# Kernel optimization log

Hardware: AMD Instinct MI355X
Metric: run time of the kernel (lower is better)

## Reference

```python
import jax, jax.numpy as jnp
import numpy as np

T, B, IN, H, OUT = 512, 256, 64, 512, 64


def setup_inputs() -> dict:
    key = jax.random.key(0)
    ks = jax.random.split(key, 12)
    s_in = 1.0 / np.sqrt(H)
    u = lambda k, shape: jax.random.uniform(k, shape, jnp.float32, -s_in, s_in)
    return {
        "x": jax.random.normal(ks[0], (T, B, IN), jnp.float32),
        # layer 0 LSTMCell params (PyTorch layout: [4H, in], gate order i,f,g,o)
        "W_ih0": u(ks[1], (4 * H, IN)),
        "W_hh0": u(ks[2], (4 * H, H)),
        "b_ih0": u(ks[3], (4 * H,)),
        "b_hh0": u(ks[4], (4 * H,)),
        # layer 1 LSTMCell params
        "W_ih1": u(ks[5], (4 * H, H)),
        "W_hh1": u(ks[6], (4 * H, H)),
        "b_ih1": u(ks[7], (4 * H,)),
        "b_hh1": u(ks[8], (4 * H,)),
        # output linear
        "W_lin": u(ks[9], (OUT, H)),
        "b_lin": u(ks[10], (OUT,)),
        "future": 0,
    }


def _lstm_cell(x_t, h, c, Wi, Wh, bi, bh):
    # gates: [B, 4H], PyTorch order i, f, g, o
    g = x_t @ Wi.T + bi + h @ Wh.T + bh
    i, f, gg, o = jnp.split(g, 4, axis=-1)
    c_new = jax.nn.sigmoid(f) * c + jax.nn.sigmoid(i) * jnp.tanh(gg)
    h_new = jax.nn.sigmoid(o) * jnp.tanh(c_new)
    return h_new, c_new


def reference(x, W_ih0, W_hh0, b_ih0, b_hh0, W_ih1, W_hh1, b_ih1, b_hh1,
              W_lin, b_lin, future):
    Bs = x.shape[1]
    h0 = jnp.zeros((Bs, H), x.dtype)
    init = (h0, h0, h0, h0)  # h_t[0], c_t[0], h_t[1], c_t[1]

    def step(carry, x_t):
        h_0, c_0, h_1, c_1 = carry
        h_0, c_0 = _lstm_cell(x_t, h_0, c_0, W_ih0, W_hh0, b_ih0, b_hh0)
        h_1, c_1 = _lstm_cell(h_0, h_1, c_1, W_ih1, W_hh1, b_ih1, b_hh1)
        out = h_1 @ W_lin.T + b_lin  # dropout is identity in eval mode
        return (h_0, c_0, h_1, c_1), out

    carry, outs = jax.lax.scan(step, init, x)  # outs: [T, B, OUT]

    if future > 0:
        def fstep(state, _):
            (h_0, c_0, h_1, c_1), out = state
            h_0, c_0 = _lstm_cell(out, h_0, c_0, W_ih0, W_hh0, b_ih0, b_hh0)
            h_1, c_1 = _lstm_cell(h_0, h_1, c_1, W_ih1, W_hh1, b_ih1, b_hh1)
            out = h_1 @ W_lin.T + b_lin
            return ((h_0, c_0, h_1, c_1), out), out
        _, fouts = jax.lax.scan(fstep, (carry, outs[-1]), None, length=future)
        outs = jnp.concatenate([outs, fouts], axis=0)

    # torch.cat(outputs, dim=1): [B, (T+future)*OUT]
    return jnp.transpose(outs, (1, 0, 2)).reshape(Bs, -1)
```

## Files before the change

### kernel.cpp

```cpp
#include <hip/hip_runtime.h>
#include <hip/hip_bf16.h>

#define TT  512
#define BB  256
#define IND 64
#define HH  512
#define OD  64
#define BBHH (BB * HH)
#define NSLOT 8
#define FSTRIDE 32
#define XSTR  133
#define XSTR0 261

typedef __bf16 v8bf  __attribute__((ext_vector_type(8)));
typedef float  v4f   __attribute__((ext_vector_type(4)));
typedef float  v16f  __attribute__((ext_vector_type(16)));


struct Params {
  const __bf16 *xb, *Wi0, *Wh0, *Wi1, *Wh1, *Wlin;
  const float  *bsum0, *bsum1, *blin;
  __bf16 *h0, *h1;
  int *flags;
  float *out;
};

__device__ __forceinline__ float sigm(float x) { return 1.f / (1.f + __expf(-x)); }
__device__ __forceinline__ float tanh_fast(float x) {
  float e = __expf(2.f * x);
  return 1.f - 2.f / (e + 1.f);
}
__device__ __forceinline__ v4f mfma16(v8bf a, v8bf b, v4f c) {
  return __builtin_amdgcn_mfma_f32_16x16x32_bf16(a, b, c, 0, 0, 0);
}
__device__ __forceinline__ v16f mfma32(v8bf a, v8bf b, v16f c) {
  return __builtin_amdgcn_mfma_f32_32x32x16_bf16(a, b, c, 0, 0, 0);
}
__device__ __forceinline__ v8bf bc(v4f x) { return __builtin_bit_cast(v8bf, x); }

__device__ __forceinline__ void ldsload16(const __bf16* g, __bf16* l) {
  __builtin_amdgcn_global_load_lds(
      (const __attribute__((address_space(1))) void*)(const void*)g,
      (__attribute__((address_space(3))) void*)(void*)l,
      16, 0, 17);
}
__device__ __forceinline__ void vwait() {
  asm volatile("s_waitcnt vmcnt(0)" ::: "memory");
}
__device__ __forceinline__ void astore8(unsigned long long* p, unsigned long long v) {
  __hip_atomic_store(p, v, __ATOMIC_RELAXED, __HIP_MEMORY_SCOPE_AGENT);
}
__device__ __forceinline__ void pollOne(const int* p, int target) {
  while (__hip_atomic_load(p, __ATOMIC_RELAXED, __HIP_MEMORY_SCOPE_AGENT) < target)
    __builtin_amdgcn_s_sleep(1);
}
__device__ __forceinline__ void drainAll() {
  asm volatile("s_waitcnt vmcnt(0)" ::: "memory");
  __syncthreads();
}
__device__ __forceinline__ void setFlag(int* f, int v) {
  if (threadIdx.x == 0)
    __hip_atomic_store(f, v, __ATOMIC_RELAXED, __HIP_MEMORY_SCOPE_AGENT);
}

__global__ void __launch_bounds__(256) prep_kernel(
    const float* x, const float* Wi0, const float* Wh0, const float* bi0, const float* bh0,
    const float* Wi1, const float* Wh1, const float* bi1, const float* bh1, const float* Wlin,
    __bf16* xb, __bf16* Wi0b, __bf16* Wh0b, __bf16* Wi1b, __bf16* Wh1b, __bf16* Wlinb,
    float* bsum0, float* bsum1, __bf16* h0, __bf16* h1, int* flags) {
  size_t tid = (size_t)blockIdx.x * blockDim.x + threadIdx.x;
  size_t np  = (size_t)gridDim.x * blockDim.x;
  for (size_t i = tid; i < (size_t)TT * BB * IND; i += np) xb[i]    = (__bf16)x[i];
  for (size_t i = tid; i < (size_t)4 * HH * IND;  i += np) Wi0b[i]  = (__bf16)Wi0[i];
  for (size_t i = tid; i < (size_t)4 * HH * HH;   i += np) Wh0b[i]  = (__bf16)Wh0[i];
  for (size_t i = tid; i < (size_t)4 * HH * HH;   i += np) Wi1b[i]  = (__bf16)Wi1[i];
  for (size_t i = tid; i < (size_t)4 * HH * HH;   i += np) Wh1b[i]  = (__bf16)Wh1[i];
  for (size_t i = tid; i < (size_t)OD * HH;       i += np) Wlinb[i] = (__bf16)Wlin[i];
  for (size_t i = tid; i < (size_t)4 * HH; i += np) {
    bsum0[i] = bi0[i] + bh0[i];
    bsum1[i] = bi1[i] + bh1[i];
  }
  for (size_t i = tid; i < (size_t)NSLOT * BBHH; i += np) { h0[i] = (__bf16)0.f; h1[i] = (__bf16)0.f; }
  for (size_t i = tid; i < (size_t)200 * FSTRIDE; i += np)
    __hip_atomic_store(&flags[i], 0, __ATOMIC_RELAXED, __HIP_MEMORY_SCOPE_AGENT);
}

__global__ void __launch_bounds__(256, 1) lstm_persist(Params P) {
  __shared__ __align__(16) __bf16 sA[32 * 128 * 8];
  __shared__ __align__(16) float  xch[32 * XSTR0];

  const int bid  = blockIdx.x;
  const int tid  = threadIdx.x;
  const int lane = tid & 63;
  const int wid  = tid >> 6;
  const int khi  = lane >> 5;
  const int l32  = lane & 31;
  const int g    = bid & 7;
  const int k    = bid >> 3;
  int* FL = P.flags;
  const int m0 = g * 32;

  if (k >= 8 && k < 24) {
    const int j  = k - 8;
    const int j0 = j * 32;
    const int n  = wid * HH + j0 + l32;
    v4f breg[64];
    {
      const __bf16* Wh = P.Wh1 + (size_t)n * HH + khi * 8;
      #pragma unroll
      for (int ks = 0; ks < 32; ++ks) breg[ks]      = *(const v4f*)(Wh + ks * 16);
      const __bf16* Wi = P.Wi1 + (size_t)n * HH + khi * 8;
      #pragma unroll
      for (int ks = 0; ks < 32; ++ks) breg[32 + ks] = *(const v4f*)(Wi + ks * 16);
      #pragma unroll
      for (int i = 0; i < 64; ++i) asm volatile("" : "+v"(breg[i]));
    }
    const int er = tid & 31, ecg = tid >> 5;
    const int jc = j0 + ecg * 4;
    const v4f bI = *(const v4f*)(P.bsum1 + jc);
    const v4f bF = *(const v4f*)(P.bsum1 + HH + jc);
    const v4f bG = *(const v4f*)(P.bsum1 + 2 * HH + jc);
    const v4f bO = *(const v4f*)(P.bsum1 + 3 * HH + jc);
    float creg[4] = {0.f, 0.f, 0.f, 0.f};
    const int hsw = l32 & 7;
    const __bf16* abase = sA + (size_t)l32 * 128 * 8;

    for (int t = 0; t < TT; ++t) {
      if (tid < 16)       pollOne(FL + (64 + g * 16 + tid) * FSTRIDE, t);
      else if (tid < 24)  pollOne(FL + (g * 8 + (tid - 16)) * FSTRIDE, t + 1);
      else if (tid == 24) pollOne(FL + (192 + g) * FSTRIDE, t - 7);
      __syncthreads();
      {
        const __bf16* s1 = P.h1 + (size_t)((t + NSLOT - 1) & (NSLOT - 1)) * BBHH + (size_t)m0 * HH;
        const __bf16* s0 = P.h0 + (size_t)(t & (NSLOT - 1)) * BBHH + (size_t)m0 * HH;
        #pragma unroll
        for (int rr = 0; rr < 8; ++rr) {
          const int r  = wid * 8 + rr;
          const int cc = lane ^ (r & 7);
          ldsload16(s1 + (size_t)r * HH + cc * 8, sA + ((size_t)r * 128) * 8);
          ldsload16(s0 + (size_t)r * HH + cc * 8, sA + ((size_t)r * 128 + 64) * 8);
        }
        vwait();
      }
      __syncthreads();
      v16f a0 = {0,0,0,0,0,0,0,0,0,0,0,0,0,0,0,0};
      v16f a1 = {0,0,0,0,0,0,0,0,0,0,0,0,0,0,0,0};
      #pragma unroll
      for (int ks = 0; ks < 64; ks += 2) {
        v8bf af0 = *(const v8bf*)(abase + (((ks    ) * 2 + khi) ^ hsw) * 8);
        a0 = mfma32(af0, bc(breg[ks]), a0);
        v8bf af1 = *(const v8bf*)(abase + (((ks + 1) * 2 + khi) ^ hsw) * 8);
        a1 = mfma32(af1, bc(breg[ks + 1]), a1);
      }
      #pragma unroll
      for (int rg = 0; rg < 16; ++rg) {
        int row = (rg & 3) + 8 * (rg >> 2) + 4 * khi;
        xch[row * XSTR + wid * 32 + l32] = a0[rg] + a1[rg];
      }
      __syncthreads();
      {
        const float* xr = xch + er * XSTR + ecg * 4;
        v4f vi = *(const v4f*)(xr);
        v4f vf = *(const v4f*)(xr + 32);
        v4f vg = *(const v4f*)(xr + 64);
        v4f vo = *(const v4f*)(xr + 96);
        unsigned long long pk = 0;
        #pragma unroll
        for (int q = 0; q < 4; ++q) {
          float cn = sigm(vf[q] + bF[q]) * creg[q] + sigm(vi[q] + bI[q]) * tanh_fast(vg[q] + bG[q]);
          creg[q] = cn;
          __bf16 hb = (__bf16)(sigm(vo[q] + bO[q]) * tanh_fast(cn));
          pk |= (unsigned long long)__builtin_bit_cast(unsigned short, hb) << (16 * q);
        }
        astore8((unsigned long long*)(P.h1 + (size_t)(t & (NSLOT - 1)) * BBHH
                                      + (size_t)(m0 + er) * HH + jc), pk);
      }
      drainAll();
      setFlag(FL + (64 + g * 16 + j) * FSTRIDE, t + 1);
    }
  } else if (k < 8) {
    const int j  = k;
    const int nA = wid * HH + j * 64 + l32;
    const int nB = nA + 32;
    v4f bregA[36], bregB[36];
    {
      const __bf16* WiA = P.Wi0 + (size_t)nA * IND + khi * 8;
      const __bf16* WiB = P.Wi0 + (size_t)nB * IND + khi * 8;
      #pragma unroll
      for (int ks = 0; ks < 4; ++ks) {
        bregA[ks] = *(const v4f*)(WiA + ks * 16);
        bregB[ks] = *(const v4f*)(WiB + ks * 16);
      }
      const __bf16* WhA = P.Wh0 + (size_t)nA * HH + khi * 8;
      const __bf16* WhB = P.Wh0 + (size_t)nB * HH + khi * 8;
      #pragma unroll
      for (int ks = 0; ks < 32; ++ks) {
        bregA[4 + ks] = *(const v4f*)(WhA + ks * 16);
        bregB[4 + ks] = *(const v4f*)(WhB + ks * 16);
      }
      #pragma unroll
      for (int i = 0; i < 36; ++i) {
        asm volatile("" : "+v"(bregA[i]));
        asm volatile("" : "+v"(bregB[i]));
      }
    }
    const int er = tid & 31, ec8 = tid >> 5;
    const int jc = j * 64 + ec8 * 8;
    float creg[8] = {0.f,0.f,0.f,0.f,0.f,0.f,0.f,0.f};
    const int hsw = l32 & 7;
    const __bf16* abase = sA + (size_t)l32 * 72 * 8;

    for (int t = 0; t < TT; ++t) {
      if (tid < 8)       pollOne(FL + (g * 8 + tid) * FSTRIDE, t);
      else if (tid < 24) pollOne(FL + (64 + g * 16 + (tid - 8)) * FSTRIDE, t - 7);
      __syncthreads();
      const __bf16* h0src = P.h0 + (size_t)((t + NSLOT - 1) & (NSLOT - 1)) * BBHH;
      __bf16*       hdst  = P.h0 + (size_t)(t & (NSLOT - 1)) * BBHH;
      {
        const __bf16* hs = h0src + (size_t)m0 * HH;
        #pragma unroll
        for (int rr = 0; rr < 8; ++rr) {
          const int r  = wid * 8 + rr;
          const int cc = lane ^ (r & 7);
          ldsload16(hs + (size_t)r * HH + cc * 8, sA + ((size_t)r * 72 + 8) * 8);
        }
        const int xrow = tid >> 3, xcc = tid & 7;
        v8bf tx = *(const v8bf*)(P.xb + (size_t)t * BB * IND
                                 + (size_t)(m0 + xrow) * IND + xcc * 8);
        *(v8bf*)(sA + ((size_t)xrow * 72 + (xcc ^ (xrow & 7))) * 8) = tx;
        vwait();
      }
      __syncthreads();
      v16f accA = {0,0,0,0,0,0,0,0,0,0,0,0,0,0,0,0};
      v16f accB = {0,0,0,0,0,0,0,0,0,0,0,0,0,0,0,0};
      #pragma unroll
      for (int ks = 0; ks < 36; ++ks) {
        v8bf af = *(const v8bf*)(abase + (((ks << 1) + khi) ^ hsw) * 8);
        accA = mfma32(af, bc(bregA[ks]), accA);
        accB = mfma32(af, bc(bregB[ks]), accB);
      }
      #pragma unroll
      for (int rg = 0; rg < 16; ++rg) {
        int row = (rg & 3) + 8 * (rg >> 2) + 4 * khi;
        xch[row * XSTR0 + wid * 64 + l32]      = accA[rg];
        xch[row * XSTR0 + wid * 64 + 32 + l32] = accB[rg];
      }
      __syncthreads();
      {
        const float* xr = xch + er * XSTR0 + ec8 * 8;
        #pragma unroll
        for (int p = 0; p < 2; ++p) {
          const int cb = jc + p * 4;
          v4f vi = *(const v4f*)(xr + p * 4);
          v4f vf = *(const v4f*)(xr + 64 + p * 4);
          v4f vg = *(const v4f*)(xr + 128 + p * 4);
          v4f vo = *(const v4f*)(xr + 192 + p * 4);
          v4f bI = *(const v4f*)(P.bsum0 + cb);
          v4f bF = *(const v4f*)(P.bsum0 + HH + cb);
          v4f bG = *(const v4f*)(P.bsum0 + 2 * HH + cb);
          v4f bO = *(const v4f*)(P.bsum0 + 3 * HH + cb);
          unsigned long long pk = 0;
          #pragma unroll
          for (int q = 0; q < 4; ++q) {
            float cn = sigm(vf[q] + bF[q]) * creg[p * 4 + q]
                     + sigm(vi[q] + bI[q]) * tanh_fast(vg[q] + bG[q]);
            creg[p * 4 + q] = cn;
            __bf16 hb = (__bf16)(sigm(vo[q] + bO[q]) * tanh_fast(cn));
            pk |= (unsigned long long)__builtin_bit_cast(unsigned short, hb) << (16 * q);
          }
          astore8((unsigned long long*)(hdst + (size_t)(m0 + er) * HH + cb), pk);
        }
      }
      drainAll();
      setFlag(FL + (g * 8 + j) * FSTRIDE, t + 1);
    }
  } else {
    const int l16 = lane & 15, quad = lane >> 4;
    const int col = wid * 16 + l16;
    v4f breg[16];
    {
      const __bf16* W = P.Wlin + (size_t)col * HH + quad * 8;
      #pragma unroll
      for (int kk = 0; kk < 16; ++kk) breg[kk] = *(const v4f*)(W + kk * 32);
      #pragma unroll
      for (int i = 0; i < 16; ++i) asm volatile("" : "+v"(breg[i]));
    }
    const float bb = P.blin[col];
    for (int t = 0; t < TT; ++t) {
      if (tid < 16) pollOne(FL + (64 + g * 16 + tid) * FSTRIDE, t + 1);
      __syncthreads();
      {
        const __bf16* src = P.h1 + (size_t)(t & (NSLOT - 1)) * BBHH + (size_t)m0 * HH;
        #pragma unroll
        for (int rr = 0; rr < 8; ++rr) {
          const int r  = wid * 8 + rr;
          const int cc = lane ^ (r & 7);
          ldsload16(src + (size_t)r * HH + cc * 8, sA + ((size_t)r * 64) * 8);
        }
        vwait();
      }
      __syncthreads();
      setFlag(FL + (192 + g) * FSTRIDE, t + 1);
      v4f acc0 = {0.f,0.f,0.f,0.f}, acc1 = {0.f,0.f,0.f,0.f};
      #pragma unroll
      for (int kk = 0; kk < 16; ++kk) {
        int c8 = kk * 4 + quad;
        int r0 = l16, r1 = 16 + l16;
        v8bf af0 = *(const v8bf*)(sA + ((size_t)r0 * 64 + (c8 ^ (r0 & 7))) * 8);
        acc0 = mfma16(af0, bc(breg[kk]), acc0);
        v8bf af1 = *(const v8bf*)(sA + ((size_t)r1 * 64 + (c8 ^ (r1 & 7))) * 8);
        acc1 = mfma16(af1, bc(breg[kk]), acc1);
      }
      #pragma unroll
      for (int r = 0; r < 4; ++r) {
        int b0r = m0 + quad * 4 + r;
        P.out[(size_t)b0r * (TT * OD) + (size_t)t * OD + col] = acc0[r] + bb;
        int b1r = m0 + 16 + quad * 4 + r;
        P.out[(size_t)b1r * (TT * OD) + (size_t)t * OD + col] = acc1[r] + bb;
      }
    }
  }
}

extern "C" void kernel_launch(void* const* d_in, const int* in_sizes, int n_in,
                              void* d_out, int out_size, void* d_ws, size_t ws_size,
                              hipStream_t stream) {
  const float* x    = (const float*)d_in[0];
  const float* Wi0  = (const float*)d_in[1];
  const float* Wh0  = (const float*)d_in[2];
  const float* bi0  = (const float*)d_in[3];
  const float* bh0  = (const float*)d_in[4];
  const float* Wi1  = (const float*)d_in[5];
  const float* Wh1  = (const float*)d_in[6];
  const float* bi1  = (const float*)d_in[7];
  const float* bh1  = (const float*)d_in[8];
  const float* Wlin = (const float*)d_in[9];
  const float* blin = (const float*)d_in[10];

  char* base = (char*)d_ws;
  size_t off = 0;
  auto take = [&](size_t nbytes) {
    void* p = base + off;
    off = (off + nbytes + 255) & ~(size_t)255;
    return p;
  };
  __bf16* xb    = (__bf16*)take(sizeof(__bf16) * (size_t)TT * BB * IND);
  __bf16* Wi0b  = (__bf16*)take(sizeof(__bf16) * 4 * HH * IND);
  __bf16* Wh0b  = (__bf16*)take(sizeof(__bf16) * 4 * HH * HH);
  __bf16* Wi1b  = (__bf16*)take(sizeof(__bf16) * 4 * HH * HH);
  __bf16* Wh1b  = (__bf16*)take(sizeof(__bf16) * 4 * HH * HH);
  __bf16* Wlinb = (__bf16*)take(sizeof(__bf16) * OD * HH);
  float*  bsum0 = (float*)take(sizeof(float) * 4 * HH);
  float*  bsum1 = (float*)take(sizeof(float) * 4 * HH);
  __bf16* h0    = (__bf16*)take(sizeof(__bf16) * NSLOT * BBHH);
  __bf16* h1    = (__bf16*)take(sizeof(__bf16) * NSLOT * BBHH);
  int*    flags = (int*)take(sizeof(int) * 200 * FSTRIDE);

  prep_kernel<<<dim3(1024), dim3(256), 0, stream>>>(
      x, Wi0, Wh0, bi0, bh0, Wi1, Wh1, bi1, bh1, Wlin,
      xb, Wi0b, Wh0b, Wi1b, Wh1b, Wlinb, bsum0, bsum1, h0, h1, flags);

  Params P;
  P.xb = xb; P.Wi0 = Wi0b; P.Wh0 = Wh0b; P.Wi1 = Wi1b; P.Wh1 = Wh1b; P.Wlin = Wlinb;
  P.bsum0 = bsum0; P.bsum1 = bsum1; P.blin = blin;
  P.h0 = h0; P.h1 = h1;
  P.flags = flags;
  P.out = (float*)d_out;

  void* kargs[] = { (void*)&P };
  hipError_t err = hipLaunchCooperativeKernel(reinterpret_cast<void*>(lstm_persist),
                                              dim3(200), dim3(256), kargs, 0, stream);
  if (err != hipSuccess) {
    lstm_persist<<<dim3(200), dim3(256), 0, stream>>>(P);
  }
}
```

Measured before the change: 3.292 ms.

## Use XCD-local cache scope for h exchange when each group shares one XCD

At startup every block records its XCD id and waits at a grid-wide arrival counter, then checks whether all 25 blocks of its batch group g landed on the same XCD. If so, h loads into LDS use cache policy 1 instead of 17 and h stores use workgroup scope instead of agent scope, so exchanges can stay in the XCD-local L2 and skip device-coherent traffic. Output stores also become nontemporal. The added startup barrier costs some time. Correctness depends on the cache-coherence assumptions holding across CUs within one XCD.

After: 2.945 ms. -10.5%, faster.

```diff
diff --git a/kernel.cpp b/kernel.cpp
--- a/kernel.cpp
+++ b/kernel.cpp
@@ -22,6 +22,8 @@
   const float  *bsum0, *bsum1, *blin;
   __bf16 *h0, *h1;
   int *flags;
+  int *xcdmap;
+  int *ready;
   float *out;
 };
 
@@ -38,17 +40,26 @@
 }
 __device__ __forceinline__ v8bf bc(v4f x) { return __builtin_bit_cast(v8bf, x); }
 
-__device__ __forceinline__ void ldsload16(const __bf16* g, __bf16* l) {
-  __builtin_amdgcn_global_load_lds(
-      (const __attribute__((address_space(1))) void*)(const void*)g,
-      (__attribute__((address_space(3))) void*)(void*)l,
-      16, 0, 17);
+template<bool LOCAL>
+__device__ __forceinline__ void ldsload16T(const __bf16* g, __bf16* l) {
+  if constexpr (LOCAL)
+    __builtin_amdgcn_global_load_lds(
+        (const __attribute__((address_space(1))) void*)(const void*)g,
+        (__attribute__((address_space(3))) void*)(void*)l, 16, 0, 1);
+  else
+    __builtin_amdgcn_global_load_lds(
+        (const __attribute__((address_space(1))) void*)(const void*)g,
+        (__attribute__((address_space(3))) void*)(void*)l, 16, 0, 17);
 }
 __device__ __forceinline__ void vwait() {
   asm volatile("s_waitcnt vmcnt(0)" ::: "memory");
 }
-__device__ __forceinline__ void astore8(unsigned long long* p, unsigned long long v) {
-  __hip_atomic_store(p, v, __ATOMIC_RELAXED, __HIP_MEMORY_SCOPE_AGENT);
+template<bool LOCAL>
+__device__ __forceinline__ void astore8T(unsigned long long* p, unsigned long long v) {
+  if constexpr (LOCAL)
+    __hip_atomic_store(p, v, __ATOMIC_RELAXED, __HIP_MEMORY_SCOPE_WORKGROUP);
+  else
+    __hip_atomic_store(p, v, __ATOMIC_RELAXED, __HIP_MEMORY_SCOPE_AGENT);
 }
 __device__ __forceinline__ void pollOne(const int* p, int target) {
   while (__hip_atomic_load(p, __ATOMIC_RELAXED, __HIP_MEMORY_SCOPE_AGENT) < target)
@@ -67,7 +78,7 @@
     const float* x, const float* Wi0, const float* Wh0, const float* bi0, const float* bh0,
     const float* Wi1, const float* Wh1, const float* bi1, const float* bh1, const float* Wlin,
     __bf16* xb, __bf16* Wi0b, __bf16* Wh0b, __bf16* Wi1b, __bf16* Wh1b, __bf16* Wlinb,
-    float* bsum0, float* bsum1, __bf16* h0, __bf16* h1, int* flags) {
+    float* bsum0, float* bsum1, __bf16* h0, __bf16* h1, int* flags, int* ready) {
   size_t tid = (size_t)blockIdx.x * blockDim.x + threadIdx.x;
   size_t np  = (size_t)gridDim.x * blockDim.x;
   for (size_t i = tid; i < (size_t)TT * BB * IND; i += np) xb[i]    = (__bf16)x[i];
@@ -83,14 +94,12 @@
   for (size_t i = tid; i < (size_t)NSLOT * BBHH; i += np) { h0[i] = (__bf16)0.f; h1[i] = (__bf16)0.f; }
   for (size_t i = tid; i < (size_t)200 * FSTRIDE; i += np)
     __hip_atomic_store(&flags[i], 0, __ATOMIC_RELAXED, __HIP_MEMORY_SCOPE_AGENT);
-}
-
-__global__ void __launch_bounds__(256, 1) lstm_persist(Params P) {
-  __shared__ __align__(16) __bf16 sA[32 * 128 * 8];
-  __shared__ __align__(16) float  xch[32 * XSTR0];
-
-  const int bid  = blockIdx.x;
-  const int tid  = threadIdx.x;
+  if (tid == 0) *ready = 0;
+}
+
+template<bool LOCAL>
+__device__ __forceinline__ void persist_body(const Params& P, int bid, int tid,
+                                             __bf16* sA, float* xch) {
   const int lane = tid & 63;
   const int wid  = tid >> 6;
   const int khi  = lane >> 5;
@@ -137,8 +146,8 @@
         for (int rr = 0; rr < 8; ++rr) {
           const int r  = wid * 8 + rr;
           const int cc = lane ^ (r & 7);
-          ldsload16(s1 + (size_t)r * HH + cc * 8, sA + ((size_t)r * 128) * 8);
-          ldsload16(s0 + (size_t)r * HH + cc * 8, sA + ((size_t)r * 128 + 64) * 8);
+          ldsload16T<LOCAL>(s1 + (size_t)r * HH + cc * 8, sA + ((size_t)r * 128) * 8);
+          ldsload16T<LOCAL>(s0 + (size_t)r * HH + cc * 8, sA + ((size_t)r * 128 + 64) * 8);
         }
         vwait();
       }
@@ -172,8 +181,8 @@
           __bf16 hb = (__bf16)(sigm(vo[q] + bO[q]) * tanh_fast(cn));
           pk |= (unsigned long long)__builtin_bit_cast(unsigned short, hb) << (16 * q);
         }
-        astore8((unsigned long long*)(P.h1 + (size_t)(t & (NSLOT - 1)) * BBHH
-                                      + (size_t)(m0 + er) * HH + jc), pk);
+        astore8T<LOCAL>((unsigned long long*)(P.h1 + (size_t)(t & (NSLOT - 1)) * BBHH
+                                              + (size_t)(m0 + er) * HH + jc), pk);
       }
       drainAll();
       setFlag(FL + (64 + g * 16 + j) * FSTRIDE, t + 1);
@@ -222,7 +231,7 @@
         for (int rr = 0; rr < 8; ++rr) {
           const int r  = wid * 8 + rr;
           const int cc = lane ^ (r & 7);
-          ldsload16(hs + (size_t)r * HH + cc * 8, sA + ((size_t)r * 72 + 8) * 8);
+          ldsload16T<LOCAL>(hs + (size_t)r * HH + cc * 8, sA + ((size_t)r * 72 + 8) * 8);
         }
         const int xrow = tid >> 3, xcc = tid & 7;
         v8bf tx = *(const v8bf*)(P.xb + (size_t)t * BB * IND
@@ -268,7 +277,7 @@
             __bf16 hb = (__bf16)(sigm(vo[q] + bO[q]) * tanh_fast(cn));
             pk |= (unsigned long long)__builtin_bit_cast(unsigned short, hb) << (16 * q);
           }
-          astore8((unsigned long long*)(hdst + (size_t)(m0 + er) * HH + cb), pk);
+          astore8T<LOCAL>((unsigned long long*)(hdst + (size_t)(m0 + er) * HH + cb), pk);
         }
       }
       drainAll();
@@ -295,7 +304,7 @@
         for (int rr = 0; rr < 8; ++rr) {
           const int r  = wid * 8 + rr;
           const int cc = lane ^ (r & 7);
-          ldsload16(src + (size_t)r * HH + cc * 8, sA + ((size_t)r * 64) * 8);
+          ldsload16T<LOCAL>(src + (size_t)r * HH + cc * 8, sA + ((size_t)r * 64) * 8);
         }
         vwait();
       }
@@ -314,12 +323,51 @@
       #pragma unroll
       for (int r = 0; r < 4; ++r) {
         int b0r = m0 + quad * 4 + r;
-        P.out[(size_t)b0r * (TT * OD) + (size_t)t * OD + col] = acc0[r] + bb;
+        __builtin_nontemporal_store(acc0[r] + bb,
+            &P.out[(size_t)b0r * (TT * OD) + (size_t)t * OD + col]);
         int b1r = m0 + 16 + quad * 4 + r;
-        P.out[(size_t)b1r * (TT * OD) + (size_t)t * OD + col] = acc1[r] + bb;
+        __builtin_nontemporal_store(acc1[r] + bb,
+            &P.out[(size_t)b1r * (TT * OD) + (size_t)t * OD + col]);
       }
     }
   }
+}
+
+__global__ void __launch_bounds__(256, 1) lstm_persist(Params P) {
+  __shared__ __align__(16) __bf16 sA[32 * 128 * 8];
+  __shared__ __align__(16) float  xch[32 * XSTR0];
+  __shared__ int sLocal;
+
+  const int bid = blockIdx.x;
+  const int tid = threadIdx.x;
+  const int g   = bid & 7;
+
+  if (tid == 0) {
+    int xcd;
+    asm volatile("s_getreg_b32 %0, hwreg(HW_REG_XCC_ID)" : "=s"(xcd));
+    __hip_atomic_store(&P.xcdmap[bid], xcd, __ATOMIC_RELAXED, __HIP_MEMORY_SCOPE_AGENT);
+    asm volatile("s_waitcnt vmcnt(0)" ::: "memory");
+    asm volatile("buffer_inv sc0 sc1" ::: "memory");
+    __hip_atomic_fetch_add(P.ready, 1, __ATOMIC_RELAXED, __HIP_MEMORY_SCOPE_AGENT);
+    int it = 0;
+    while (__hip_atomic_load(P.ready, __ATOMIC_RELAXED, __HIP_MEMORY_SCOPE_AGENT) < 200
+           && it < 200000) {
+      __builtin_amdgcn_s_sleep(2);
+      ++it;
+    }
+    int ok = (it < 200000) ? 1 : 0;
+    if (ok) {
+      int x0 = __hip_atomic_load(&P.xcdmap[g], __ATOMIC_RELAXED, __HIP_MEMORY_SCOPE_AGENT);
+      for (int kk = 1; kk < 25; ++kk)
+        ok &= (__hip_atomic_load(&P.xcdmap[g + 8 * kk], __ATOMIC_RELAXED,
+                                 __HIP_MEMORY_SCOPE_AGENT) == x0);
+    }
+    sLocal = ok;
+  }
+  __syncthreads();
+
+  if (sLocal) persist_body<true>(P, bid, tid, sA, xch);
+  else        persist_body<false>(P, bid, tid, sA, xch);
 }
 
 extern "C" void kernel_launch(void* const* d_in, const int* in_sizes, int n_in,
@@ -355,16 +403,19 @@
   __bf16* h0    = (__bf16*)take(sizeof(__bf16) * NSLOT * BBHH);
   __bf16* h1    = (__bf16*)take(sizeof(__bf16) * NSLOT * BBHH);
   int*    flags = (int*)take(sizeof(int) * 200 * FSTRIDE);
+  int*    xcdmap= (int*)take(sizeof(int) * 256);
+  int*    ready = (int*)take(sizeof(int) * 64);
 
   prep_kernel<<<dim3(1024), dim3(256), 0, stream>>>(
       x, Wi0, Wh0, bi0, bh0, Wi1, Wh1, bi1, bh1, Wlin,
-      xb, Wi0b, Wh0b, Wi1b, Wh1b, Wlinb, bsum0, bsum1, h0, h1, flags);
+      xb, Wi0b, Wh0b, Wi1b, Wh1b, Wlinb, bsum0, bsum1, h0, h1, flags, ready);
 
   Params P;
   P.xb = xb; P.Wi0 = Wi0b; P.Wh0 = Wh0b; P.Wi1 = Wi1b; P.Wh1 = Wh1b; P.Wlin = Wlinb;
   P.bsum0 = bsum0; P.bsum1 = bsum1; P.blin = blin;
   P.h0 = h0; P.h1 = h1;
   P.flags = flags;
+  P.xcdmap = xcdmap; P.ready = ready;
   P.out = (float*)d_out;
 
   void* kargs[] = { (void*)&P };
```
